# Optimization experiments

Measured on AMD Instinct MI355X. Metric: run time of the kernel, lower is better.

Reference implementation:

```python
import jax, jax.numpy as jnp
import numpy as np

B, T, C = 2, 2048, 2048
N_HEAD, N_KV_HEAD = 16, 4
HEAD_DIM = C // N_HEAD  # 128
EPS = 1e-6


def rms_norm(x):
    # no learned scale, normalize over head_dim (last axis)
    return x * jax.lax.rsqrt(jnp.mean(jnp.square(x), axis=-1, keepdims=True) + EPS)


def apply_rotary_emb(x, cos, sin):
    # x: [B, T, H, D]; cos/sin: [T, D/2]  (rotate-half RoPE)
    x1, x2 = jnp.split(x, 2, axis=-1)
    c = cos[None, :, None, :]
    s = sin[None, :, None, :]
    return jnp.concatenate([x1 * c - x2 * s, x1 * s + x2 * c], axis=-1)


def setup_inputs() -> dict:
    key = jax.random.key(0)
    ks = jax.random.split(key, 6)
    x = jax.random.normal(ks[0], (B, T, C), dtype=jnp.float32)
    # real rotary tables: theta = 10000^{-2i/D}
    inv_freq = 1.0 / (10000.0 ** (jnp.arange(0, HEAD_DIM, 2, dtype=jnp.float32) / HEAD_DIM))
    angles = jnp.arange(T, dtype=jnp.float32)[:, None] * inv_freq[None, :]  # [T, D/2]
    cos, sin = jnp.cos(angles), jnp.sin(angles)
    std = 0.02
    Wq = jax.random.normal(ks[1], (C, N_HEAD * HEAD_DIM), dtype=jnp.float32) * std
    Wk = jax.random.normal(ks[2], (C, N_KV_HEAD * HEAD_DIM), dtype=jnp.float32) * std
    Wv = jax.random.normal(ks[3], (C, N_KV_HEAD * HEAD_DIM), dtype=jnp.float32) * std
    Wp = jax.random.normal(ks[4], (C, C), dtype=jnp.float32) * std
    return {"x": x, "cos": cos, "sin": sin, "Wq": Wq, "Wk": Wk, "Wv": Wv, "Wp": Wp}


def reference(x, cos, sin, Wq, Wk, Wv, Wp):
    Bx, Tx, Cx = x.shape
    q = (x @ Wq).reshape(Bx, Tx, N_HEAD, HEAD_DIM)
    k = (x @ Wk).reshape(Bx, Tx, N_KV_HEAD, HEAD_DIM)
    v = (x @ Wv).reshape(Bx, Tx, N_KV_HEAD, HEAD_DIM)
    q = rms_norm(apply_rotary_emb(q, cos, sin))
    k = rms_norm(apply_rotary_emb(k, cos, sin))
    # module scales q by 1/sqrt(D) AND nn.dot_product_attention scales again
    q = q * (1.0 / jnp.sqrt(HEAD_DIM))
    # GQA head repeat
    n_rep = N_HEAD // N_KV_HEAD
    k = jnp.repeat(k, n_rep, axis=2)  # [B, T, H, D]
    v = jnp.repeat(v, n_rep, axis=2)
    scores = jnp.einsum("bthd,bshd->bhts", q, k) / jnp.sqrt(jnp.asarray(HEAD_DIM, x.dtype))
    causal = jnp.tril(jnp.ones((Tx, Tx), dtype=bool))  # key <= query
    scores = jnp.where(causal[None, None, :, :], scores, jnp.finfo(scores.dtype).min)
    probs = jax.nn.softmax(scores, axis=-1)
    y = jnp.einsum("bhts,bshd->bthd", probs, v).reshape(Bx, Tx, Cx)
    return y @ Wp
```

## Files before the change

kernel.cpp:

```cpp
#include <hip/hip_runtime.h>
#include <hip/hip_bf16.h>
#include <math.h>

#define B_  2
#define T_  2048
#define C_  2048
#define NH_ 16
#define NKV_ 4
#define HD_ 128
#define NREP_ (NH_/NKV_)

#define QKVLD 3072
#define KOFF  2048
#define VOFF  2560

#define QSCALE 0.01127105500694502f

typedef __bf16 bf16x8 __attribute__((ext_vector_type(8)));
typedef float  f32x4  __attribute__((ext_vector_type(4)));

__device__ inline void gload_lds16(const void* g, void* l) {
    __builtin_amdgcn_global_load_lds((const __attribute__((address_space(1))) void*)g,
                                     (__attribute__((address_space(3))) void*)l, 16, 0, 0);
}

__global__ __launch_bounds__(256) void cast_bf16(const float* __restrict__ src,
                                                 __bf16* __restrict__ dst)
{
    size_t i = ((size_t)blockIdx.x * 256 + threadIdx.x) * 8;
    float4 a = *(const float4*)&src[i];
    float4 b = *(const float4*)&src[i + 4];
    union { __bf16 h[8]; uint4 u; } pk;
    pk.h[0] = (__bf16)a.x; pk.h[1] = (__bf16)a.y; pk.h[2] = (__bf16)a.z; pk.h[3] = (__bf16)a.w;
    pk.h[4] = (__bf16)b.x; pk.h[5] = (__bf16)b.y; pk.h[6] = (__bf16)b.z; pk.h[7] = (__bf16)b.w;
    *(uint4*)&dst[i] = pk.u;
}

__global__ __launch_bounds__(256) void wtrans_qkv(const float* __restrict__ Wq,
                                                  const float* __restrict__ Wk,
                                                  const float* __restrict__ Wv,
                                                  __bf16* __restrict__ dst)
{
    __shared__ float tl[32][33];
    int ct = blockIdx.x;
    int k0 = blockIdx.y * 32;
    const float* src;
    int ncols, c0, dr0;
    if (ct < 64)      { src = Wq; ncols = 2048; c0 = ct * 32;        dr0 = ct * 32; }
    else if (ct < 80) { src = Wk; ncols = 512;  c0 = (ct - 64) * 32; dr0 = KOFF + (ct - 64) * 32; }
    else              { src = Wv; ncols = 512;  c0 = (ct - 80) * 32; dr0 = VOFF + (ct - 80) * 32; }

    int tid = threadIdx.x;
    int r  = tid >> 3;
    int c4 = (tid & 7) * 4;
    float4 v = *(const float4*)&src[(size_t)(k0 + r) * ncols + c0 + c4];
    tl[r][c4] = v.x; tl[r][c4 + 1] = v.y; tl[r][c4 + 2] = v.z; tl[r][c4 + 3] = v.w;
    __syncthreads();
    union { __bf16 h[4]; uint2 u; } pk;
#pragma unroll
    for (int j = 0; j < 4; ++j) pk.h[j] = (__bf16)tl[c4 + j][r];
    *(uint2*)&dst[(size_t)(dr0 + r) * 2048 + k0 + c4] = pk.u;
}

__global__ __launch_bounds__(256) void wtrans(const float* __restrict__ src,
                                              __bf16* __restrict__ dst, int ncols)
{
    __shared__ float tl[32][33];
    int n0 = blockIdx.x * 32;
    int k0 = blockIdx.y * 32;
    int tid = threadIdx.x;
    int r  = tid >> 3;
    int c4 = (tid & 7) * 4;
    float4 v = *(const float4*)&src[(size_t)(k0 + r) * ncols + n0 + c4];
    tl[r][c4] = v.x; tl[r][c4 + 1] = v.y; tl[r][c4 + 2] = v.z; tl[r][c4 + 3] = v.w;
    __syncthreads();
    union { __bf16 h[4]; uint2 u; } pk;
#pragma unroll
    for (int j = 0; j < 4; ++j) pk.h[j] = (__bf16)tl[c4 + j][r];
    *(uint2*)&dst[(size_t)(n0 + r) * 2048 + k0 + c4] = pk.u;
}

template<typename TOUT>
__global__ __launch_bounds__(256) void gemm_bt(const __bf16* __restrict__ A,
                                               const __bf16* __restrict__ Bt,
                                               TOUT* __restrict__ C,
                                               int M, int N, int K, int ldc)
{
    __shared__ __bf16 As[2][128 * 32];
    __shared__ __bf16 Bs[2][128 * 32];

    const int tid  = threadIdx.x;
    const int wv   = tid >> 6;
    const int lane = tid & 63;
    const int grp  = lane >> 4;
    const int id16 = lane & 15;
    const int wr   = wv >> 1;
    const int wc   = wv & 1;

    const int row0 = blockIdx.y * 128;
    const int col0 = blockIdx.x * 128;

    const int sm = tid >> 2;
    const int sk = (tid & 3) << 3;

    const __bf16* ga0 = A  + (size_t)(row0 + sm) * K + sk;
    const __bf16* ga1 = A  + (size_t)(row0 + 64 + sm) * K + sk;
    const __bf16* gb0 = Bt + (size_t)(col0 + sm) * K + sk;
    const __bf16* gb1 = Bt + (size_t)(col0 + 64 + sm) * K + sk;

    f32x4 acc[4][4];
    const f32x4 fz = {0.f, 0.f, 0.f, 0.f};
#pragma unroll
    for (int i = 0; i < 4; ++i)
#pragma unroll
        for (int j = 0; j < 4; ++j) acc[i][j] = fz;

    const int nk = K >> 5;

    {
        __bf16* a0 = &As[0][wv << 9];
        __bf16* b0 = &Bs[0][wv << 9];
        gload_lds16(ga0, a0);
        gload_lds16(ga1, a0 + 2048);
        gload_lds16(gb0, b0);
        gload_lds16(gb1, b0 + 2048);
    }

    for (int kt = 0; kt < nk; ++kt) {
        const int bufc = kt & 1;
        asm volatile("s_waitcnt vmcnt(0)" ::: "memory");
        __syncthreads();

        if (kt + 1 < nk) {
            const int kb = (kt + 1) << 5;
            __bf16* a0 = &As[1 - bufc][wv << 9];
            __bf16* b0 = &Bs[1 - bufc][wv << 9];
            gload_lds16(ga0 + kb, a0);
            gload_lds16(ga1 + kb, a0 + 2048);
            gload_lds16(gb0 + kb, b0);
            gload_lds16(gb1 + kb, b0 + 2048);
        }

        bf16x8 af[4], bfr[4];
#pragma unroll
        for (int i = 0; i < 4; ++i)
            af[i] = *(const bf16x8*)&As[bufc][((wr << 6) + (i << 4) + id16) * 32 + (grp << 3)];
#pragma unroll
        for (int j = 0; j < 4; ++j)
            bfr[j] = *(const bf16x8*)&Bs[bufc][((wc << 6) + (j << 4) + id16) * 32 + (grp << 3)];
#pragma unroll
        for (int i = 0; i < 4; ++i)
#pragma unroll
            for (int j = 0; j < 4; ++j)
                acc[i][j] = __builtin_amdgcn_mfma_f32_16x16x32_bf16(af[i], bfr[j], acc[i][j], 0, 0, 0);
    }

#pragma unroll
    for (int i = 0; i < 4; ++i) {
        int gr = row0 + (wr << 6) + (i << 4) + (grp << 2);
#pragma unroll
        for (int j = 0; j < 4; ++j) {
            int gc = col0 + (wc << 6) + (j << 4) + id16;
#pragma unroll
            for (int r = 0; r < 4; ++r) {
                if constexpr (sizeof(TOUT) == 4)
                    C[(size_t)(gr + r) * ldc + gc] = acc[i][j][r];
                else
                    C[(size_t)(gr + r) * ldc + gc] = (TOUT)acc[i][j][r];
            }
        }
    }
}

__global__ __launch_bounds__(256) void rope_rms_b(__bf16* __restrict__ base,
                                                  const float* __restrict__ cosb,
                                                  const float* __restrict__ sinb,
                                                  int nheads, float scale)
{
    int wid  = blockIdx.x * 4 + (threadIdx.x >> 6);
    int lane = threadIdx.x & 63;
    int bt = wid / nheads;
    int hd = wid % nheads;
    int t  = bt % T_;

    __bf16* p = base + (size_t)bt * QKVLD + hd * HD_;
    float c = cosb[t * 64 + lane];
    float s = sinb[t * 64 + lane];
    float x1 = (float)p[lane];
    float x2 = (float)p[lane + 64];
    float r1 = x1 * c - x2 * s;
    float r2 = x1 * s + x2 * c;
    float ss = r1 * r1 + r2 * r2;
#pragma unroll
    for (int off = 32; off; off >>= 1) ss += __shfl_xor(ss, off, 64);
    float inv = rsqrtf(ss * (1.f / 128.f) + 1e-6f) * scale;
    p[lane]      = (__bf16)(r1 * inv);
    p[lane + 64] = (__bf16)(r2 * inv);
}

__global__ __launch_bounds__(256) void vtrans(const __bf16* __restrict__ qkv,
                                              __bf16* __restrict__ vt)
{
    __shared__ __bf16 tl[32][HD_ + 8];
    int bx  = blockIdx.x;
    int st  = bx & 63;
    int bkv = bx >> 6;
    int b = bkv >> 2, kv = bkv & 3;
    int s0 = st << 5;
    int tid = threadIdx.x;
    {
        int s = tid >> 3;
        int d = (tid & 7) << 4;
        const __bf16* src = qkv + (size_t)(b * T_ + s0 + s) * QKVLD + VOFF + kv * HD_ + d;
        *(bf16x8*)&tl[s][d]     = *(const bf16x8*)src;
        *(bf16x8*)&tl[s][d + 8] = *(const bf16x8*)(src + 8);
    }
    __syncthreads();
    {
        int d  = tid >> 1;
        int sh = (tid & 1) << 4;
        __bf16 tmp[16];
#pragma unroll
        for (int j = 0; j < 16; ++j) tmp[j] = tl[sh + j][d];
        __bf16* dst = vt + ((size_t)(b * NKV_ + kv) * HD_ + d) * T_ + s0 + sh;
        *(bf16x8*)dst       = *(bf16x8*)&tmp[0];
        *(bf16x8*)(dst + 8) = *(bf16x8*)&tmp[8];
    }
}

#define KT2 64
#define PP  72

__global__ __launch_bounds__(256) void attn_mfma2(const __bf16* __restrict__ qkv,
                                                  const __bf16* __restrict__ vbT,
                                                  __bf16* __restrict__ y)
{
    __shared__ __bf16 Ks[2][KT2 * 128];
    __shared__ __bf16 VTs[2][128 * KT2];
    __shared__ __bf16 Ps[4][16 * PP];

    const int tid  = threadIdx.x;
    const int wv   = tid >> 6;
    const int lane = tid & 63;
    const int grp  = lane >> 4;
    const int id16 = lane & 15;

    const int bx = blockIdx.x;
    const int j  = bx & 15;
    const int bh = bx >> 4;
    const int b  = bh >> 4;
    const int h  = bh & 15;
    const int kv = h >> 2;

    const int q0a = j << 6;
    const int q0b = (31 - j) << 6;
    const int NTa = j + 1;
    const int NT  = 33;

    const int l4 = lane >> 4, l8 = lane >> 3;
    size_t koff[4], voff[4];
#pragma unroll
    for (int i = 0; i < 4; ++i) {
        int key = wv * 16 + i * 4 + l4;
        int ch  = (lane & 15) ^ (i * 4 + l4);
        koff[i] = (size_t)key * (QKVLD * 2) + ch * 16;
        int d   = wv * 32 + i * 8 + l8;
        int ch2 = (lane & 7) ^ l8;
        voff[i] = (size_t)d * (T_ * 2) + ch2 * 16;
    }
    const char* kg = (const char*)(qkv + (size_t)b * T_ * QKVLD + KOFF + kv * HD_);
    const char* vg = (const char*)(vbT + ((size_t)(b * NKV_ + kv) * HD_) * T_);

    bf16x8 qf[4], qf2[4];
    {
        const __bf16* qp = qkv + (size_t)(b * T_ + q0a + wv * 16 + id16) * QKVLD + h * HD_ + (grp << 3);
#pragma unroll
        for (int c = 0; c < 4; ++c) qf[c] = *(const bf16x8*)(qp + c * 32);
        const __bf16* qp2 = qkv + (size_t)(b * T_ + q0b + wv * 16 + id16) * QKVLD + h * HD_ + (grp << 3);
#pragma unroll
        for (int c = 0; c < 4; ++c) qf2[c] = *(const bf16x8*)(qp2 + c * 32);
    }

    const f32x4 fz = {0.f, 0.f, 0.f, 0.f};
    f32x4 o[8];
#pragma unroll
    for (int c = 0; c < 8; ++c) o[c] = fz;
    float l_r[4];
#pragma unroll
    for (int r = 0; r < 4; ++r) l_r[r] = 0.f;

    int qbase = q0a + wv * 16;
    int q0c   = q0a;

    {
        __bf16* kl = &Ks[0][(wv * 16) * 128];
        __bf16* vl = &VTs[0][(wv * 32) * 64];
#pragma unroll
        for (int i = 0; i < 4; ++i) gload_lds16(kg + koff[i], kl + i * 4 * 128);
#pragma unroll
        for (int i = 0; i < 4; ++i) gload_lds16(vg + voff[i], vl + i * 8 * 64);
    }

    for (int tt = 0; tt < NT; ++tt) {
        const int bufc = tt & 1;
        asm volatile("s_waitcnt vmcnt(0)" ::: "memory");
        __syncthreads();

        if (tt + 1 < NT) {
            int tn = tt + 1;
            int sn = (tn >= NTa ? tn - NTa : tn) << 6;
            __bf16* kl = &Ks[tn & 1][(wv * 16) * 128];
            __bf16* vl = &VTs[tn & 1][(wv * 32) * 64];
            const char* kp = kg + (size_t)sn * (QKVLD * 2);
            const char* vp = vg + (size_t)sn * 2;
#pragma unroll
            for (int i = 0; i < 4; ++i) gload_lds16(kp + koff[i], kl + i * 4 * 128);
#pragma unroll
            for (int i = 0; i < 4; ++i) gload_lds16(vp + voff[i], vl + i * 8 * 64);
        }

        if (tt == NTa) {
            float inv[4];
#pragma unroll
            for (int r = 0; r < 4; ++r) {
                float l = l_r[r];
                l += __shfl_xor(l, 1, 64);
                l += __shfl_xor(l, 2, 64);
                l += __shfl_xor(l, 4, 64);
                l += __shfl_xor(l, 8, 64);
                inv[r] = 1.f / l;
            }
#pragma unroll
            for (int r = 0; r < 4; ++r) {
                int q = qbase + (grp << 2) + r;
                __bf16* yp = y + (size_t)(b * T_ + q) * C_ + h * HD_ + id16;
#pragma unroll
                for (int c = 0; c < 8; ++c) yp[c * 16] = (__bf16)(o[c][r] * inv[r]);
            }
#pragma unroll
            for (int c = 0; c < 8; ++c) o[c] = fz;
#pragma unroll
            for (int r = 0; r < 4; ++r) l_r[r] = 0.f;
#pragma unroll
            for (int c = 0; c < 4; ++c) qf[c] = qf2[c];
            qbase = q0b + wv * 16;
            q0c   = q0b;
        }

        const int s0 = (tt >= NTa ? tt - NTa : tt) << 6;

        f32x4 S[4];
#pragma unroll
        for (int t = 0; t < 4; ++t) S[t] = fz;
#pragma unroll
        for (int c = 0; c < 4; ++c) {
#pragma unroll
            for (int t = 0; t < 4; ++t) {
                bf16x8 kf = *(const bf16x8*)&Ks[bufc][(t * 16 + id16) * 128 + ((((c << 2) + grp) ^ id16) << 3)];
                S[t] = __builtin_amdgcn_mfma_f32_16x16x32_bf16(qf[c], kf, S[t], 0, 0, 0);
            }
        }
        if (s0 == q0c) {
#pragma unroll
            for (int t = 0; t < 4; ++t)
#pragma unroll
                for (int r = 0; r < 4; ++r)
                    if (s0 + t * 16 + id16 > qbase + (grp << 2) + r) S[t][r] = -1e30f;
        }

#pragma unroll
        for (int t = 0; t < 4; ++t)
#pragma unroll
            for (int r = 0; r < 4; ++r) S[t][r] = exp2f(S[t][r]);
#pragma unroll
        for (int r = 0; r < 4; ++r)
            l_r[r] += (S[0][r] + S[1][r]) + (S[2][r] + S[3][r]);

        __bf16* pw = Ps[wv];
#pragma unroll
        for (int t = 0; t < 4; ++t)
#pragma unroll
            for (int r = 0; r < 4; ++r)
                pw[((grp << 2) + r) * PP + t * 16 + id16] = (__bf16)S[t][r];

        asm volatile("s_waitcnt lgkmcnt(0)" ::: "memory");
        bf16x8 pf0 = *(const bf16x8*)&pw[id16 * PP + (grp << 3)];
        bf16x8 pf1 = *(const bf16x8*)&pw[id16 * PP + 32 + (grp << 3)];

#pragma unroll
        for (int c2 = 0; c2 < 8; ++c2) {
            bf16x8 vf0 = *(const bf16x8*)&VTs[bufc][(c2 * 16 + id16) * 64 + ((grp ^ (id16 & 7)) << 3)];
            o[c2] = __builtin_amdgcn_mfma_f32_16x16x32_bf16(pf0, vf0, o[c2], 0, 0, 0);
            bf16x8 vf1 = *(const bf16x8*)&VTs[bufc][(c2 * 16 + id16) * 64 + (((4 + grp) ^ (id16 & 7)) << 3)];
            o[c2] = __builtin_amdgcn_mfma_f32_16x16x32_bf16(pf1, vf1, o[c2], 0, 0, 0);
        }
    }

    {
        float inv[4];
#pragma unroll
        for (int r = 0; r < 4; ++r) {
            float l = l_r[r];
            l += __shfl_xor(l, 1, 64);
            l += __shfl_xor(l, 2, 64);
            l += __shfl_xor(l, 4, 64);
            l += __shfl_xor(l, 8, 64);
            inv[r] = 1.f / l;
        }
#pragma unroll
        for (int r = 0; r < 4; ++r) {
            int q = qbase + (grp << 2) + r;
            __bf16* yp = y + (size_t)(b * T_ + q) * C_ + h * HD_ + id16;
#pragma unroll
            for (int c = 0; c < 8; ++c) yp[c * 16] = (__bf16)(o[c][r] * inv[r]);
        }
    }
}

extern "C" void kernel_launch(void* const* d_in, const int* in_sizes, int n_in,
                              void* d_out, int out_size, void* d_ws, size_t ws_size,
                              hipStream_t stream)
{
    const float* x    = (const float*)d_in[0];
    const float* cosb = (const float*)d_in[1];
    const float* sinb = (const float*)d_in[2];
    const float* Wq   = (const float*)d_in[3];
    const float* Wk   = (const float*)d_in[4];
    const float* Wv   = (const float*)d_in[5];
    const float* Wp   = (const float*)d_in[6];
    float* out = (float*)d_out;

    const int M = B_ * T_;

    char* w = (char*)d_ws;
    __bf16* xb    = (__bf16*)w;  w += (size_t)M * C_ * 2;
    __bf16* qkv   = (__bf16*)w;  w += (size_t)M * QKVLD * 2;
    __bf16* wqkvT = (__bf16*)w;  w += (size_t)QKVLD * C_ * 2;
    __bf16* wpT   = (__bf16*)w;  w += (size_t)C_ * C_ * 2;
    __bf16* vt    = (__bf16*)w;  w += (size_t)M * NKV_ * HD_ * 2;
    __bf16* y     = (__bf16*)w;

    cast_bf16<<<(M * C_) / 2048, 256, 0, stream>>>(x, xb);
    wtrans_qkv<<<dim3(96, C_ / 32), 256, 0, stream>>>(Wq, Wk, Wv, wqkvT);
    wtrans<<<dim3(C_ / 32, C_ / 32), 256, 0, stream>>>(Wp, wpT, C_);

    gemm_bt<__bf16><<<dim3(QKVLD / 128, M / 128), 256, 0, stream>>>(xb, wqkvT, qkv, M, QKVLD, C_, QKVLD);

    rope_rms_b<<<(M * NH_) / 4, 256, 0, stream>>>(qkv, cosb, sinb, NH_, QSCALE);
    rope_rms_b<<<(M * NKV_) / 4, 256, 0, stream>>>(qkv + KOFF, cosb, sinb, NKV_, 1.0f);

    vtrans<<<B_ * NKV_ * (T_ / 32), 256, 0, stream>>>(qkv, vt);

    attn_mfma2<<<B_ * NH_ * 16, 256, 0, stream>>>(qkv, vt, y);

    gemm_bt<float><<<dim3(C_ / 128, M / 128), 256, 0, stream>>>(y, wpT, out, M, C_, C_, C_);
}
```

Measured before the change: 320.9 us.

## Use two waves with 32 query rows each in attention to reuse K/V fragments

The attention kernel drops from four waves of 16 query rows each to two waves of 32 rows each, launched with 128 threads. Each K and V fragment read from LDS now feeds two MFMAs, which halves LDS read traffic per MFMA. The second Q tile is loaded lazily rather than held in registers, and the diagonal mask uses a tile-local comparison. In exchange, each block has half as many threads to issue the global-to-LDS copies and more accumulator registers per wave, which can reduce latency hiding.

```diff
diff --git a/kernel.cpp b/kernel.cpp
--- a/kernel.cpp
+++ b/kernel.cpp
@@ -231,13 +231,13 @@
 #define KT2 64
 #define PP  72
 
-__global__ __launch_bounds__(256) void attn_mfma2(const __bf16* __restrict__ qkv,
-                                                  const __bf16* __restrict__ vbT,
-                                                  __bf16* __restrict__ y)
+__global__ __launch_bounds__(128, 1) void attn_mfma3(const __bf16* __restrict__ qkv,
+                                                     const __bf16* __restrict__ vbT,
+                                                     __bf16* __restrict__ y)
 {
     __shared__ __bf16 Ks[2][KT2 * 128];
     __shared__ __bf16 VTs[2][128 * KT2];
-    __shared__ __bf16 Ps[4][16 * PP];
+    __shared__ __bf16 Ps[2][32 * PP];
 
     const int tid  = threadIdx.x;
     const int wv   = tid >> 6;
@@ -258,47 +258,50 @@
     const int NT  = 33;
 
     const int l4 = lane >> 4, l8 = lane >> 3;
-    size_t koff[4], voff[4];
-#pragma unroll
-    for (int i = 0; i < 4; ++i) {
-        int key = wv * 16 + i * 4 + l4;
-        int ch  = (lane & 15) ^ (i * 4 + l4);
-        koff[i] = (size_t)key * (QKVLD * 2) + ch * 16;
-        int d   = wv * 32 + i * 8 + l8;
+    unsigned koff[8], voff[8];
+#pragma unroll
+    for (int i = 0; i < 8; ++i) {
+        int key = wv * 32 + i * 4 + l4;
+        int ch  = (lane & 15) ^ ((i * 4 + l4) & 15);
+        koff[i] = (unsigned)key * (QKVLD * 2) + ch * 16;
+        int d   = wv * 64 + i * 8 + l8;
         int ch2 = (lane & 7) ^ l8;
-        voff[i] = (size_t)d * (T_ * 2) + ch2 * 16;
+        voff[i] = (unsigned)d * (T_ * 2) + ch2 * 16;
     }
     const char* kg = (const char*)(qkv + (size_t)b * T_ * QKVLD + KOFF + kv * HD_);
     const char* vg = (const char*)(vbT + ((size_t)(b * NKV_ + kv) * HD_) * T_);
 
-    bf16x8 qf[4], qf2[4];
+    bf16x8 qf[2][4];
     {
-        const __bf16* qp = qkv + (size_t)(b * T_ + q0a + wv * 16 + id16) * QKVLD + h * HD_ + (grp << 3);
-#pragma unroll
-        for (int c = 0; c < 4; ++c) qf[c] = *(const bf16x8*)(qp + c * 32);
-        const __bf16* qp2 = qkv + (size_t)(b * T_ + q0b + wv * 16 + id16) * QKVLD + h * HD_ + (grp << 3);
-#pragma unroll
-        for (int c = 0; c < 4; ++c) qf2[c] = *(const bf16x8*)(qp2 + c * 32);
+#pragma unroll
+        for (int qt = 0; qt < 2; ++qt) {
+            const __bf16* qp = qkv + (size_t)(b * T_ + q0a + wv * 32 + qt * 16 + id16) * QKVLD + h * HD_ + (grp << 3);
+#pragma unroll
+            for (int c = 0; c < 4; ++c) qf[qt][c] = *(const bf16x8*)(qp + c * 32);
+        }
     }
 
     const f32x4 fz = {0.f, 0.f, 0.f, 0.f};
-    f32x4 o[8];
-#pragma unroll
-    for (int c = 0; c < 8; ++c) o[c] = fz;
-    float l_r[4];
-#pragma unroll
-    for (int r = 0; r < 4; ++r) l_r[r] = 0.f;
-
-    int qbase = q0a + wv * 16;
-    int q0c   = q0a;
+    f32x4 o[2][8];
+#pragma unroll
+    for (int qt = 0; qt < 2; ++qt)
+#pragma unroll
+        for (int c = 0; c < 8; ++c) o[qt][c] = fz;
+    float l_acc[2][4];
+#pragma unroll
+    for (int qt = 0; qt < 2; ++qt)
+#pragma unroll
+        for (int r = 0; r < 4; ++r) l_acc[qt][r] = 0.f;
+
+    int qv  = q0a + wv * 32;
 
     {
-        __bf16* kl = &Ks[0][(wv * 16) * 128];
-        __bf16* vl = &VTs[0][(wv * 32) * 64];
-#pragma unroll
-        for (int i = 0; i < 4; ++i) gload_lds16(kg + koff[i], kl + i * 4 * 128);
-#pragma unroll
-        for (int i = 0; i < 4; ++i) gload_lds16(vg + voff[i], vl + i * 8 * 64);
+        __bf16* kl = &Ks[0][(wv * 32) * 128];
+        __bf16* vl = &VTs[0][(wv * 64) * 64];
+#pragma unroll
+        for (int i = 0; i < 8; ++i) gload_lds16(kg + koff[i], kl + i * 512);
+#pragma unroll
+        for (int i = 0; i < 8; ++i) gload_lds16(vg + voff[i], vl + i * 512);
     }
 
     for (int tt = 0; tt < NT; ++tt) {
@@ -309,112 +312,127 @@
         if (tt + 1 < NT) {
             int tn = tt + 1;
             int sn = (tn >= NTa ? tn - NTa : tn) << 6;
-            __bf16* kl = &Ks[tn & 1][(wv * 16) * 128];
-            __bf16* vl = &VTs[tn & 1][(wv * 32) * 64];
+            __bf16* kl = &Ks[tn & 1][(wv * 32) * 128];
+            __bf16* vl = &VTs[tn & 1][(wv * 64) * 64];
             const char* kp = kg + (size_t)sn * (QKVLD * 2);
             const char* vp = vg + (size_t)sn * 2;
 #pragma unroll
-            for (int i = 0; i < 4; ++i) gload_lds16(kp + koff[i], kl + i * 4 * 128);
-#pragma unroll
-            for (int i = 0; i < 4; ++i) gload_lds16(vp + voff[i], vl + i * 8 * 64);
+            for (int i = 0; i < 8; ++i) gload_lds16(kp + koff[i], kl + i * 512);
+#pragma unroll
+            for (int i = 0; i < 8; ++i) gload_lds16(vp + voff[i], vl + i * 512);
         }
 
         if (tt == NTa) {
-            float inv[4];
-#pragma unroll
-            for (int r = 0; r < 4; ++r) {
-                float l = l_r[r];
-                l += __shfl_xor(l, 1, 64);
-                l += __shfl_xor(l, 2, 64);
-                l += __shfl_xor(l, 4, 64);
-                l += __shfl_xor(l, 8, 64);
-                inv[r] = 1.f / l;
+#pragma unroll
+            for (int qt = 0; qt < 2; ++qt)
+#pragma unroll
+                for (int r = 0; r < 4; ++r) {
+                    float l = l_acc[qt][r];
+                    l += __shfl_xor(l, 1, 64);
+                    l += __shfl_xor(l, 2, 64);
+                    l += __shfl_xor(l, 4, 64);
+                    l += __shfl_xor(l, 8, 64);
+                    float inv = 1.f / l;
+                    int q = qv + qt * 16 + (grp << 2) + r;
+                    __bf16* yp = y + (size_t)(b * T_ + q) * C_ + h * HD_ + id16;
+#pragma unroll
+                    for (int c = 0; c < 8; ++c) yp[c * 16] = (__bf16)(o[qt][c][r] * inv);
+                }
+#pragma unroll
+            for (int qt = 0; qt < 2; ++qt) {
+#pragma unroll
+                for (int c = 0; c < 8; ++c) o[qt][c] = fz;
+#pragma unroll
+                for (int r = 0; r < 4; ++r) l_acc[qt][r] = 0.f;
+                const __bf16* qp = qkv + (size_t)(b * T_ + q0b + wv * 32 + qt * 16 + id16) * QKVLD + h * HD_ + (grp << 3);
+#pragma unroll
+                for (int c = 0; c < 4; ++c) qf[qt][c] = *(const bf16x8*)(qp + c * 32);
             }
-#pragma unroll
-            for (int r = 0; r < 4; ++r) {
-                int q = qbase + (grp << 2) + r;
-                __bf16* yp = y + (size_t)(b * T_ + q) * C_ + h * HD_ + id16;
-#pragma unroll
-                for (int c = 0; c < 8; ++c) yp[c * 16] = (__bf16)(o[c][r] * inv[r]);
-            }
-#pragma unroll
-            for (int c = 0; c < 8; ++c) o[c] = fz;
-#pragma unroll
-            for (int r = 0; r < 4; ++r) l_r[r] = 0.f;
-#pragma unroll
-            for (int c = 0; c < 4; ++c) qf[c] = qf2[c];
-            qbase = q0b + wv * 16;
-            q0c   = q0b;
-        }
-
-        const int s0 = (tt >= NTa ? tt - NTa : tt) << 6;
-
-        f32x4 S[4];
-#pragma unroll
-        for (int t = 0; t < 4; ++t) S[t] = fz;
+            qv = q0b + wv * 32;
+        }
+
+        const bool diag = (tt == NTa - 1) || (tt == NT - 1);
+
+        f32x4 S[2][4];
+#pragma unroll
+        for (int qt = 0; qt < 2; ++qt)
+#pragma unroll
+            for (int t = 0; t < 4; ++t) S[qt][t] = fz;
 #pragma unroll
         for (int c = 0; c < 4; ++c) {
 #pragma unroll
             for (int t = 0; t < 4; ++t) {
                 bf16x8 kf = *(const bf16x8*)&Ks[bufc][(t * 16 + id16) * 128 + ((((c << 2) + grp) ^ id16) << 3)];
-                S[t] = __builtin_amdgcn_mfma_f32_16x16x32_bf16(qf[c], kf, S[t], 0, 0, 0);
+                S[0][t] = __builtin_amdgcn_mfma_f32_16x16x32_bf16(qf[0][c], kf, S[0][t], 0, 0, 0);
+                S[1][t] = __builtin_amdgcn_mfma_f32_16x16x32_bf16(qf[1][c], kf, S[1][t], 0, 0, 0);
             }
         }
-        if (s0 == q0c) {
+        if (diag) {
+#pragma unroll
+            for (int qt = 0; qt < 2; ++qt)
+#pragma unroll
+                for (int t = 0; t < 4; ++t)
+#pragma unroll
+                    for (int r = 0; r < 4; ++r)
+                        if (t * 16 + id16 > wv * 32 + qt * 16 + (grp << 2) + r)
+                            S[qt][t][r] = -1e30f;
+        }
+
+#pragma unroll
+        for (int qt = 0; qt < 2; ++qt)
 #pragma unroll
             for (int t = 0; t < 4; ++t)
 #pragma unroll
+                for (int r = 0; r < 4; ++r) S[qt][t][r] = exp2f(S[qt][t][r]);
+#pragma unroll
+        for (int qt = 0; qt < 2; ++qt)
+#pragma unroll
+            for (int r = 0; r < 4; ++r)
+                l_acc[qt][r] += (S[qt][0][r] + S[qt][1][r]) + (S[qt][2][r] + S[qt][3][r]);
+
+        __bf16* pw = Ps[wv];
+#pragma unroll
+        for (int qt = 0; qt < 2; ++qt)
+#pragma unroll
+            for (int t = 0; t < 4; ++t)
+#pragma unroll
                 for (int r = 0; r < 4; ++r)
-                    if (s0 + t * 16 + id16 > qbase + (grp << 2) + r) S[t][r] = -1e30f;
-        }
-
-#pragma unroll
-        for (int t = 0; t < 4; ++t)
-#pragma unroll
-            for (int r = 0; r < 4; ++r) S[t][r] = exp2f(S[t][r]);
-#pragma unroll
-        for (int r = 0; r < 4; ++r)
-            l_r[r] += (S[0][r] + S[1][r]) + (S[2][r] + S[3][r]);
-
-        __bf16* pw = Ps[wv];
-#pragma unroll
-        for (int t = 0; t < 4; ++t)
-#pragma unroll
-            for (int r = 0; r < 4; ++r)
-                pw[((grp << 2) + r) * PP + t * 16 + id16] = (__bf16)S[t][r];
+                    pw[(qt * 16 + (grp << 2) + r) * PP + t * 16 + id16] = (__bf16)S[qt][t][r];
 
         asm volatile("s_waitcnt lgkmcnt(0)" ::: "memory");
-        bf16x8 pf0 = *(const bf16x8*)&pw[id16 * PP + (grp << 3)];
-        bf16x8 pf1 = *(const bf16x8*)&pw[id16 * PP + 32 + (grp << 3)];
-
-#pragma unroll
-        for (int c2 = 0; c2 < 8; ++c2) {
-            bf16x8 vf0 = *(const bf16x8*)&VTs[bufc][(c2 * 16 + id16) * 64 + ((grp ^ (id16 & 7)) << 3)];
-            o[c2] = __builtin_amdgcn_mfma_f32_16x16x32_bf16(pf0, vf0, o[c2], 0, 0, 0);
-            bf16x8 vf1 = *(const bf16x8*)&VTs[bufc][(c2 * 16 + id16) * 64 + (((4 + grp) ^ (id16 & 7)) << 3)];
-            o[c2] = __builtin_amdgcn_mfma_f32_16x16x32_bf16(pf1, vf1, o[c2], 0, 0, 0);
-        }
-    }
-
-    {
-        float inv[4];
+        bf16x8 pf[2][2];
+#pragma unroll
+        for (int qt = 0; qt < 2; ++qt)
+#pragma unroll
+            for (int c = 0; c < 2; ++c)
+                pf[qt][c] = *(const bf16x8*)&pw[(qt * 16 + id16) * PP + c * 32 + (grp << 3)];
+
+#pragma unroll
+        for (int c = 0; c < 2; ++c) {
+#pragma unroll
+            for (int dt = 0; dt < 8; ++dt) {
+                bf16x8 vf = *(const bf16x8*)&VTs[bufc][(dt * 16 + id16) * 64 + ((((c << 2) + grp) ^ (id16 & 7)) << 3)];
+                o[0][dt] = __builtin_amdgcn_mfma_f32_16x16x32_bf16(pf[0][c], vf, o[0][dt], 0, 0, 0);
+                o[1][dt] = __builtin_amdgcn_mfma_f32_16x16x32_bf16(pf[1][c], vf, o[1][dt], 0, 0, 0);
+            }
+        }
+    }
+
+#pragma unroll
+    for (int qt = 0; qt < 2; ++qt)
 #pragma unroll
         for (int r = 0; r < 4; ++r) {
-            float l = l_r[r];
+            float l = l_acc[qt][r];
             l += __shfl_xor(l, 1, 64);
             l += __shfl_xor(l, 2, 64);
             l += __shfl_xor(l, 4, 64);
             l += __shfl_xor(l, 8, 64);
-            inv[r] = 1.f / l;
-        }
-#pragma unroll
-        for (int r = 0; r < 4; ++r) {
-            int q = qbase + (grp << 2) + r;
+            float inv = 1.f / l;
+            int q = qv + qt * 16 + (grp << 2) + r;
             __bf16* yp = y + (size_t)(b * T_ + q) * C_ + h * HD_ + id16;
 #pragma unroll
-            for (int c = 0; c < 8; ++c) yp[c * 16] = (__bf16)(o[c][r] * inv[r]);
-        }
-    }
+            for (int c = 0; c < 8; ++c) yp[c * 16] = (__bf16)(o[qt][c][r] * inv);
+        }
 }
 
 extern "C" void kernel_launch(void* const* d_in, const int* in_sizes, int n_in,
@@ -451,7 +469,7 @@
 
     vtrans<<<B_ * NKV_ * (T_ / 32), 256, 0, stream>>>(qkv, vt);
 
-    attn_mfma2<<<B_ * NH_ * 16, 256, 0, stream>>>(qkv, vt, y);
+    attn_mfma3<<<B_ * NH_ * 16, 128, 0, stream>>>(qkv, vt, y);
 
     gemm_bt<float><<<dim3(C_ / 128, M / 128), 256, 0, stream>>>(y, wpT, out, M, C_, C_, C_);
 }
```

Result: slower. 343.6 us (+7.1%).
